# Optimization experiments

Hardware: AMD Instinct MI355X
Metric: run time of the kernel (lower is better)

Reference implementation:

```python
import jax, jax.numpy as jnp
import numpy as np

N = 250_000
E = 8_000_000
EPS = 1e-5


def _bn(x, gamma, beta):
    # BatchNorm1d in training mode: batch stats over dim 0, biased variance
    mu = x.mean(axis=0)
    var = x.var(axis=0)
    return (x - mu) * jax.lax.rsqrt(var + EPS) * gamma + beta


def setup_inputs() -> dict:
    key = jax.random.key(0)
    ks = jax.random.split(key, 24)
    f32 = jnp.float32
    inp = {
        'pos': jax.random.normal(ks[0], (N, 2), f32),
        'vel': jax.random.normal(ks[1], (N, 2), f32),
        'edge_index': jax.random.randint(ks[2], (2, E), 0, N, jnp.int32),
        'lin_in_w': jax.random.normal(ks[3], (4, 4), f32) * 0.5,
        'lin_in_b': jax.random.normal(ks[4], (4,), f32) * 0.1,
        'msg_w1': jax.random.normal(ks[5], (8, 8), f32) * 0.35,
        'msg_b1': jax.random.normal(ks[6], (8,), f32) * 0.1,
        'msg_g1': jax.random.uniform(ks[7], (8,), f32, 0.5, 1.5),
        'msg_be1': jax.random.normal(ks[8], (8,), f32) * 0.1,
        'msg_w2': jax.random.normal(ks[9], (8, 4), f32) * 0.35,
        'msg_b2': jax.random.normal(ks[10], (4,), f32) * 0.1,
        'msg_g2': jax.random.uniform(ks[11], (4,), f32, 0.5, 1.5),
        'msg_be2': jax.random.normal(ks[12], (4,), f32) * 0.1,
        'upd_w1': jax.random.normal(ks[13], (8, 8), f32) * 0.35,
        'upd_b1': jax.random.normal(ks[14], (8,), f32) * 0.1,
        'upd_g1': jax.random.uniform(ks[15], (8,), f32, 0.5, 1.5),
        'upd_be1': jax.random.normal(ks[16], (8,), f32) * 0.1,
        'upd_w2': jax.random.normal(ks[17], (8, 4), f32) * 0.35,
        'upd_b2': jax.random.normal(ks[18], (4,), f32) * 0.1,
        'upd_g2': jax.random.uniform(ks[19], (4,), f32, 0.5, 1.5),
        'upd_be2': jax.random.normal(ks[20], (4,), f32) * 0.1,
        'pred_w': jax.random.normal(ks[21], (4, 2), f32) * 0.5,
        'pred_b': jax.random.normal(ks[22], (2,), f32) * 0.1,
    }
    return inp


def reference(pos, vel, edge_index,
              lin_in_w, lin_in_b,
              msg_w1, msg_b1, msg_g1, msg_be1,
              msg_w2, msg_b2, msg_g2, msg_be2,
              upd_w1, upd_b1, upd_g1, upd_be1,
              upd_w2, upd_b2, upd_g2, upd_be2,
              pred_w, pred_b):
    n = pos.shape[0]
    # input projection: h = lin_in(cat(pos, vel))  -> [N, 4]
    h = jnp.concatenate([pos, vel], axis=-1) @ lin_in_w + lin_in_b

    # PyG source_to_target: j = source = edge_index[0], i = target = edge_index[1]
    src, dst = edge_index[0], edge_index[1]
    h_i = h[dst]  # [E, 4]
    h_j = h[src]  # [E, 4]

    # message MLP on cat(h_i, h_j): Linear->BN->Tanh->Linear->BN->Tanh
    m = jnp.concatenate([h_i, h_j], axis=-1)            # [E, 8]
    m = jnp.tanh(_bn(m @ msg_w1 + msg_b1, msg_g1, msg_be1))
    m = jnp.tanh(_bn(m @ msg_w2 + msg_b2, msg_g2, msg_be2))  # [E, 4]

    # zero out messages where h_i == h_j exactly (self-like edges)
    zero_diff = jnp.all(h_i == h_j, axis=1)             # [E]
    m = jnp.where(zero_diff[:, None], 0.0, m)

    # aggregate: scatter-add on first half, scatter-mean on second half
    add_out = jax.ops.segment_sum(m[:, :2], dst, num_segments=n)   # [N, 2]
    sum_out = jax.ops.segment_sum(m[:, 2:], dst, num_segments=n)   # [N, 2]
    cnt = jax.ops.segment_sum(jnp.ones((m.shape[0],), m.dtype), dst, num_segments=n)
    mean_out = sum_out / jnp.maximum(cnt, 1.0)[:, None]
    aggr = jnp.concatenate([add_out, mean_out], axis=1)  # [N, 4]

    # update MLP on cat(h, aggr)
    u = jnp.concatenate([h, aggr], axis=-1)              # [N, 8]
    u = jnp.tanh(_bn(u @ upd_w1 + upd_b1, upd_g1, upd_be1))
    u = jnp.tanh(_bn(u @ upd_w2 + upd_b2, upd_g2, upd_be2))  # [N, 4]

    return u @ pred_w + pred_b                           # [N, 2]
```

## Files before the change

### kernel.cpp

```cpp
#include <hip/hip_runtime.h>

#define EPSBN 1e-5f
#define NB 512
#define GB 256
#define CAP 18000

typedef float vf4 __attribute__((ext_vector_type(4)));
typedef _Float16 vh8 __attribute__((ext_vector_type(8)));
typedef _Float16 vh4 __attribute__((ext_vector_type(4)));
typedef unsigned int uint32;

__device__ __forceinline__ float ftanh(float x) {
    float e = __expf(2.0f * x);
    return 1.0f - 2.0f * __builtin_amdgcn_rcpf(e + 1.0f);
}

__device__ __forceinline__ float wave_sum(float v) {
#pragma unroll
    for (int off = 32; off > 0; off >>= 1) v += __shfl_down(v, off);
    return v;
}

__device__ __forceinline__ void z1_of(const float4 hi, const float4 hj,
                                      const float* __restrict__ w, const float* __restrict__ b,
                                      float* z) {
#pragma unroll
    for (int j = 0; j < 8; ++j) {
        z[j] = b[j]
             + hi.x * w[0 * 8 + j] + hi.y * w[1 * 8 + j] + hi.z * w[2 * 8 + j] + hi.w * w[3 * 8 + j]
             + hj.x * w[4 * 8 + j] + hj.y * w[5 * 8 + j] + hj.z * w[6 * 8 + j] + hj.w * w[7 * 8 + j];
    }
}

__device__ __forceinline__ void mat8x4(const float* u, const float* w,
                                       const float* b, float* z) {
#pragma unroll
    for (int c = 0; c < 4; ++c) {
        float t = b[c];
#pragma unroll
        for (int k = 0; k < 8; ++k) t += u[k] * w[k * 4 + c];
        z[c] = t;
    }
}

__device__ __forceinline__ void mat8x8(const float* u, const float* __restrict__ w,
                                       const float* __restrict__ b, float* z) {
#pragma unroll
    for (int j = 0; j < 8; ++j) {
        float t = b[j];
#pragma unroll
        for (int k = 0; k < 8; ++k) t += u[k] * w[k * 8 + j];
        z[j] = t;
    }
}

template <int NV, int NW>
__device__ __forceinline__ void block_reduce_atomics(float* a, float* __restrict__ sums) {
    __shared__ float red[NV * NW];
    int wid = threadIdx.x >> 6, lane = threadIdx.x & 63;
#pragma unroll
    for (int i = 0; i < NV; ++i) {
        float v = wave_sum(a[i]);
        if (lane == 0) red[i * NW + wid] = v;
    }
    __syncthreads();
    if (threadIdx.x < NV) {
        float v = 0.f;
#pragma unroll
        for (int k = 0; k < NW; ++k) v += red[threadIdx.x * NW + k];
        atomicAdd(&sums[threadIdx.x], v);
    }
}

__device__ __forceinline__ void fin_lds(const float* __restrict__ sums,
                                        const float* __restrict__ g, const float* __restrict__ be,
                                        int d, float inv, float* out) {
    int j = threadIdx.x;
    if (j < d) {
        float mu = sums[j] * inv;
        float var = sums[d + j] * inv - mu * mu;
        float s = g[j] * rsqrtf(var + EPSBN);
        out[j] = s;
        out[d + j] = be[j] - mu * s;
    }
    __syncthreads();
}

__device__ __forceinline__ void stats1_edge(float4 hi, float4 hj,
                                            const float* __restrict__ w1, const float* __restrict__ b1,
                                            float* a) {
    float z[8];
    z1_of(hi, hj, w1, b1, z);
#pragma unroll
    for (int j = 0; j < 8; ++j) { a[j] += z[j]; a[8 + j] += z[j] * z[j]; }
}

__device__ __forceinline__ vf4 z2_edge(float4 hi, float4 hj,
                                       const float* __restrict__ w1, const float* __restrict__ b1,
                                       const float* ss1,
                                       const float* __restrict__ w2, const float* __restrict__ b2) {
    float z[8], m1[8], z2[4];
    z1_of(hi, hj, w1, b1, z);
#pragma unroll
    for (int j = 0; j < 8; ++j) m1[j] = ftanh(z[j] * ss1[j] + ss1[8 + j]);
    mat8x4(m1, w2, b2, z2);
    vf4 r = {z2[0], z2[1], z2[2], z2[3]};
    return r;
}

__device__ __forceinline__ void stats2_edge(float4 hi, float4 hj,
                                            const float* __restrict__ w1, const float* __restrict__ b1,
                                            const float* ss1,
                                            const float* __restrict__ w2, const float* __restrict__ b2,
                                            float* a) {
    vf4 q = z2_edge(hi, hj, w1, b1, ss1, w2, b2);
    a[0] += q.x; a[4] += q.x * q.x;
    a[1] += q.y; a[5] += q.y * q.y;
    a[2] += q.z; a[6] += q.z * q.z;
    a[3] += q.w; a[7] += q.w * q.w;
}

__global__ __launch_bounds__(256) void k_h(const float* __restrict__ pos, const float* __restrict__ vel,
                                           const float* __restrict__ w, const float* __restrict__ b,
                                           float4* __restrict__ h, int n) {
    int i = blockIdx.x * blockDim.x + threadIdx.x;
    if (i >= n) return;
    float2 p = ((const float2*)pos)[i];
    float2 v = ((const float2*)vel)[i];
    float o[4];
#pragma unroll
    for (int d = 0; d < 4; ++d)
        o[d] = b[d] + p.x * w[0 * 4 + d] + p.y * w[1 * 4 + d] + v.x * w[2 * 4 + d] + v.y * w[3 * 4 + d];
    h[i] = make_float4(o[0], o[1], o[2], o[3]);
}

__global__ __launch_bounds__(256) void k_zt(const float4* __restrict__ h,
                                            const float* __restrict__ w1, const float* __restrict__ b1,
                                            vf4* __restrict__ zi, vh8* __restrict__ zjH, int n) {
    int i = blockIdx.x * blockDim.x + threadIdx.x;
    if (i >= n) return;
    float4 hv = h[i];
    float zi8[8];
    vh8 hpk;
#pragma unroll
    for (int j = 0; j < 8; ++j) {
        zi8[j] = hv.x * w1[0 * 8 + j] + hv.y * w1[1 * 8 + j] + hv.z * w1[2 * 8 + j] + hv.w * w1[3 * 8 + j];
        float zj = b1[j]
                 + hv.x * w1[4 * 8 + j] + hv.y * w1[5 * 8 + j] + hv.z * w1[6 * 8 + j] + hv.w * w1[7 * 8 + j];
        hpk[j] = (_Float16)zj;
    }
    vf4 a = {zi8[0], zi8[1], zi8[2], zi8[3]};
    vf4 b_ = {zi8[4], zi8[5], zi8[6], zi8[7]};
    zi[2 * (size_t)i] = a; zi[2 * (size_t)i + 1] = b_;
    zjH[i] = hpk;
}

__global__ __launch_bounds__(1024, 1) void k_cnt(const int* __restrict__ idx, const float4* __restrict__ h,
                                                 const float* __restrict__ w1, const float* __restrict__ b1,
                                                 uint32* __restrict__ cntmat, float* __restrict__ sums,
                                                 int E_, int T) {
    __shared__ uint32 hist[NB];
    for (int b = threadIdx.x; b < NB; b += 1024) hist[b] = 0;
    float a[16];
#pragma unroll
    for (int i = 0; i < 16; ++i) a[i] = 0.f;
    __syncthreads();
    int lo = blockIdx.x * T, hi2 = min(E_, lo + T);
    for (int e0 = lo + 4 * threadIdx.x; e0 < hi2; e0 += 4096) {
        int m = min(4, hi2 - e0);
        if (m == 4) {
            int s0 = __builtin_nontemporal_load(idx + e0);
            int s1 = __builtin_nontemporal_load(idx + e0 + 1);
            int s2 = __builtin_nontemporal_load(idx + e0 + 2);
            int s3 = __builtin_nontemporal_load(idx + e0 + 3);
            int d0 = __builtin_nontemporal_load(idx + E_ + e0);
            int d1 = __builtin_nontemporal_load(idx + E_ + e0 + 1);
            int d2 = __builtin_nontemporal_load(idx + E_ + e0 + 2);
            int d3 = __builtin_nontemporal_load(idx + E_ + e0 + 3);
            float4 hi0 = h[d0], hj0 = h[s0];
            float4 hi1 = h[d1], hj1 = h[s1];
            float4 hi2 = h[d2], hj2 = h[s2];
            float4 hi3 = h[d3], hj3 = h[s3];
            atomicAdd(&hist[d0 >> 9], 1u);
            atomicAdd(&hist[d1 >> 9], 1u);
            atomicAdd(&hist[d2 >> 9], 1u);
            atomicAdd(&hist[d3 >> 9], 1u);
            stats1_edge(hi0, hj0, w1, b1, a);
            stats1_edge(hi1, hj1, w1, b1, a);
            stats1_edge(hi2, hj2, w1, b1, a);
            stats1_edge(hi3, hj3, w1, b1, a);
        } else {
            for (int k = 0; k < m; ++k) {
                int s = __builtin_nontemporal_load(idx + e0 + k);
                int d = __builtin_nontemporal_load(idx + E_ + e0 + k);
                float4 hi = h[d], hj = h[s];
                atomicAdd(&hist[d >> 9], 1u);
                stats1_edge(hi, hj, w1, b1, a);
            }
        }
    }
    __syncthreads();
    for (int b = threadIdx.x; b < NB; b += 1024)
        cntmat[(size_t)b * GB + blockIdx.x] = hist[b];
    block_reduce_atomics<16, 16>(a, sums);
}

__device__ __forceinline__ void scan256(uint32 v, uint32* excl_out, uint32* total) {
    __shared__ uint32 ts[256];
    ts[threadIdx.x] = v;
    __syncthreads();
    for (int off = 1; off < 256; off <<= 1) {
        uint32 t = (threadIdx.x >= (uint32)off) ? ts[threadIdx.x - off] : 0u;
        __syncthreads();
        ts[threadIdx.x] += t;
        __syncthreads();
    }
    *excl_out = ts[threadIdx.x] - v;
    *total = ts[255];
}

__device__ __forceinline__ void scan512(uint32* v, uint32* excl_out, uint32* total) {
    __shared__ uint32 ts[256];
    uint32 local = v[0] + v[1];
    ts[threadIdx.x] = local;
    __syncthreads();
    for (int off = 1; off < 256; off <<= 1) {
        uint32 t = (threadIdx.x >= (uint32)off) ? ts[threadIdx.x - off] : 0u;
        __syncthreads();
        ts[threadIdx.x] += t;
        __syncthreads();
    }
    *excl_out = ts[threadIdx.x] - local;
    *total = ts[255];
}

__global__ __launch_bounds__(256) void k_scanA(uint32* __restrict__ cntmat, uint32* __restrict__ rowtot) {
    size_t base = (size_t)blockIdx.x * GB + threadIdx.x;
    uint32 v = cntmat[base];
    uint32 excl, tot;
    scan256(v, &excl, &tot);
    cntmat[base] = excl;
    if (threadIdx.x == 0) rowtot[blockIdx.x] = tot;
}

__global__ __launch_bounds__(256) void k_scanB(const uint32* __restrict__ rowtot, uint32* __restrict__ bbase) {
    uint32 v[2];
    v[0] = rowtot[threadIdx.x * 2]; v[1] = rowtot[threadIdx.x * 2 + 1];
    uint32 excl, tot;
    scan512(v, &excl, &tot);
    bbase[threadIdx.x * 2] = excl;
    bbase[threadIdx.x * 2 + 1] = excl + v[0];
    if (threadIdx.x == 0) bbase[NB] = tot;
}

__global__ __launch_bounds__(1024, 1) void k_reorder(const int* __restrict__ idx,
                                                     const uint32* __restrict__ cntmat, const uint32* __restrict__ bbase,
                                                     uint32* __restrict__ sp, int E_, int T) {
    __shared__ uint32 cur[NB];
    for (int b = threadIdx.x; b < NB; b += 1024)
        cur[b] = bbase[b] + cntmat[(size_t)b * GB + blockIdx.x];
    __syncthreads();
    int lo = blockIdx.x * T, hi2 = min(E_, lo + T);
    for (int e0 = lo + 4 * threadIdx.x; e0 < hi2; e0 += 4096) {
        int m = min(4, hi2 - e0);
        if (m == 4) {
            int s0 = __builtin_nontemporal_load(idx + e0);
            int s1 = __builtin_nontemporal_load(idx + e0 + 1);
            int s2 = __builtin_nontemporal_load(idx + e0 + 2);
            int s3 = __builtin_nontemporal_load(idx + e0 + 3);
            int d0 = __builtin_nontemporal_load(idx + E_ + e0);
            int d1 = __builtin_nontemporal_load(idx + E_ + e0 + 1);
            int d2 = __builtin_nontemporal_load(idx + E_ + e0 + 2);
            int d3 = __builtin_nontemporal_load(idx + E_ + e0 + 3);
            uint32 p0 = atomicAdd(&cur[d0 >> 9], 1u);
            uint32 p1 = atomicAdd(&cur[d1 >> 9], 1u);
            uint32 p2 = atomicAdd(&cur[d2 >> 9], 1u);
            uint32 p3 = atomicAdd(&cur[d3 >> 9], 1u);
            sp[p0] = ((uint32)(d0 & 511) << 23) | (uint32)s0;
            sp[p1] = ((uint32)(d1 & 511) << 23) | (uint32)s1;
            sp[p2] = ((uint32)(d2 & 511) << 23) | (uint32)s2;
            sp[p3] = ((uint32)(d3 & 511) << 23) | (uint32)s3;
        } else {
            for (int k = 0; k < m; ++k) {
                int s = __builtin_nontemporal_load(idx + e0 + k);
                int d = __builtin_nontemporal_load(idx + E_ + e0 + k);
                uint32 pos = atomicAdd(&cur[d >> 9], 1u);
                sp[pos] = ((uint32)(d & 511) << 23) | (uint32)s;
            }
        }
    }
}

__global__ __launch_bounds__(256) void k_sort2(const uint32* __restrict__ sp,
                                               const uint32* __restrict__ bbase, const uint32* __restrict__ rowtot,
                                               int* __restrict__ src2, uint32* __restrict__ nodeoff, int n) {
    extern __shared__ uint32 buf[];
    __shared__ uint32 hist[512];
    __shared__ uint32 cur[512];
    int b = blockIdx.x;
    uint32 start = bbase[b];
    uint32 len = rowtot[b];
    uint32 end = start + len;
    hist[threadIdx.x] = 0;
    hist[threadIdx.x + 256] = 0;
    __syncthreads();
    for (uint32 e = start + threadIdx.x; e < end; e += 256) {
        uint32 pk = __builtin_nontemporal_load(&sp[e]);
        atomicAdd(&hist[pk >> 23], 1u);
    }
    __syncthreads();
    uint32 vv[2];
    vv[0] = hist[2 * threadIdx.x];
    vv[1] = hist[2 * threadIdx.x + 1];
    uint32 excl, tot;
    scan512(vv, &excl, &tot);
    cur[2 * threadIdx.x] = excl;
    cur[2 * threadIdx.x + 1] = excl + vv[0];
    int nodebase = b << 9;
    int node0 = nodebase + 2 * threadIdx.x;
    if (node0 <= n)     nodeoff[node0] = start + excl;
    if (node0 + 1 <= n) nodeoff[node0 + 1] = start + excl + vv[0];
    __syncthreads();
    for (uint32 e = start + threadIdx.x; e < end; e += 256) {
        uint32 pk = __builtin_nontemporal_load(&sp[e]);
        uint32 pos = atomicAdd(&cur[pk >> 23], 1u);
        uint32 src = pk & 0x7FFFFFu;
        if (pos < (uint32)CAP) buf[pos] = src;
        else src2[start + pos] = (int)src;
    }
    __syncthreads();
    uint32 lim = min(len, (uint32)CAP);
    for (uint32 k = threadIdx.x; k < lim; k += 256)
        src2[start + k] = (int)buf[k];
}

__global__ void k_fin(const float* __restrict__ sums, float* __restrict__ ss,
                      const float* __restrict__ g, const float* __restrict__ be,
                      int d, float inv_count) {
    int j = threadIdx.x;
    if (j >= d) return;
    float mu = sums[j] * inv_count;
    float var = sums[d + j] * inv_count - mu * mu;
    float s = g[j] * rsqrtf(var + EPSBN);
    ss[j] = s;
    ss[d + j] = be[j] - mu * s;
}

__global__ __launch_bounds__(256) void k_fold(vf4* __restrict__ zi, const float* __restrict__ ss1g, int n) {
    __shared__ float s[16];
    if (threadIdx.x < 16) s[threadIdx.x] = ss1g[threadIdx.x];
    __syncthreads();
    int i = blockIdx.x * blockDim.x + threadIdx.x;
    if (i >= n) return;
    vf4 a = zi[2 * (size_t)i], b = zi[2 * (size_t)i + 1];
    a.x = a.x * s[0] + s[8];  a.y = a.y * s[1] + s[9];
    a.z = a.z * s[2] + s[10]; a.w = a.w * s[3] + s[11];
    b.x = b.x * s[4] + s[12]; b.y = b.y * s[5] + s[13];
    b.z = b.z * s[6] + s[14]; b.w = b.w * s[7] + s[15];
    zi[2 * (size_t)i] = a; zi[2 * (size_t)i + 1] = b;
}

__global__ __launch_bounds__(256, 2) void e_pass2(const int* __restrict__ src2, const uint32* __restrict__ nodeoff,
                                                  const vf4* __restrict__ ziS, const vh8* __restrict__ zjH,
                                                  const float* __restrict__ ss1g,
                                                  const float* __restrict__ w2, const float* __restrict__ b2,
                                                  float* __restrict__ sums2, vh4* __restrict__ z2h, int n) {
    __shared__ float w2l[32];
    __shared__ float b2l[4];
    __shared__ float st[8];
    if (threadIdx.x < 32) w2l[threadIdx.x] = w2[threadIdx.x];
    if (threadIdx.x < 4)  b2l[threadIdx.x] = b2[threadIdx.x];
    if (threadIdx.x < 8)  st[threadIdx.x] = ss1g[threadIdx.x];
    __syncthreads();
    float a[8];
#pragma unroll
    for (int i = 0; i < 8; ++i) a[i] = 0.f;
    int lane = threadIdx.x & 15;
    int gid0 = (blockIdx.x * 256 + threadIdx.x) >> 4;
    int gstride = (gridDim.x * 256) >> 4;
    for (int i = gid0; i < n; i += gstride) {
        uint32 e0 = nodeoff[i], e1 = nodeoff[i + 1];
        vf4 ziA = ziS[2 * (size_t)i], ziB = ziS[2 * (size_t)i + 1];
        float zi8[8] = {ziA.x, ziA.y, ziA.z, ziA.w, ziB.x, ziB.y, ziB.z, ziB.w};
        uint32 e = e0 + lane;
        for (; e + 16 < e1; e += 32) {
            int sA = src2[e];
            int sB = src2[e + 16];
            vh8 ja = zjH[sA];
            vh8 jb = zjH[sB];
            float mA[8], mB[8], zA[4], zB[4];
#pragma unroll
            for (int c = 0; c < 8; ++c) {
                mA[c] = ftanh(zi8[c] + st[c] * (float)ja[c]);
                mB[c] = ftanh(zi8[c] + st[c] * (float)jb[c]);
            }
            mat8x4(mA, w2l, b2l, zA);
            mat8x4(mB, w2l, b2l, zB);
#pragma unroll
            for (int c = 0; c < 4; ++c) {
                a[c] += zA[c] + zB[c];
                a[4 + c] += zA[c] * zA[c] + zB[c] * zB[c];
            }
            vh4 pa, pb2;
            pa[0] = (sA == i) ? (_Float16)__builtin_inff() : (_Float16)zA[0];
            pa[1] = (_Float16)zA[1];
            pa[2] = (_Float16)zA[2];
            pa[3] = (_Float16)zA[3];
            pb2[0] = (sB == i) ? (_Float16)__builtin_inff() : (_Float16)zB[0];
            pb2[1] = (_Float16)zB[1];
            pb2[2] = (_Float16)zB[2];
            pb2[3] = (_Float16)zB[3];
            z2h[e] = pa;
            z2h[e + 16] = pb2;
        }
        if (e < e1) {
            int s = src2[e];
            vh8 zjh = zjH[s];
            float m1[8], z2[4];
#pragma unroll
            for (int c = 0; c < 8; ++c)
                m1[c] = ftanh(zi8[c] + st[c] * (float)zjh[c]);
            mat8x4(m1, w2l, b2l, z2);
#pragma unroll
            for (int c = 0; c < 4; ++c) {
                a[c] += z2[c];
                a[4 + c] += z2[c] * z2[c];
            }
            vh4 pk;
            pk[0] = (s == i) ? (_Float16)__builtin_inff() : (_Float16)z2[0];
            pk[1] = (_Float16)z2[1];
            pk[2] = (_Float16)z2[2];
            pk[3] = (_Float16)z2[3];
            z2h[e] = pk;
        }
    }
    block_reduce_atomics<8, 4>(a, sums2);
}

__global__ __launch_bounds__(256, 2) void e_aggr_z(const vh4* __restrict__ z2h, const uint32* __restrict__ nodeoff,
                                                   const float* __restrict__ sums2,
                                                   const float* __restrict__ g2, const float* __restrict__ be2,
                                                   float invE,
                                                   float* __restrict__ acc, int n) {
    __shared__ float ss2[8];
    fin_lds(sums2, g2, be2, 4, invE, ss2);
    int lane = threadIdx.x & 15;
    int gid0 = (blockIdx.x * 256 + threadIdx.x) >> 4;
    int gstride = (gridDim.x * 256) >> 4;
    for (int i = gid0; i < n; i += gstride) {
        uint32 e0 = nodeoff[i], e1 = nodeoff[i + 1];
        float a0 = 0.f, a1 = 0.f, a2 = 0.f, a3 = 0.f;
        uint32 e = e0 + lane;
        for (; e + 16 < e1; e += 32) {
            vh4 pa = z2h[e];
            vh4 pb = z2h[e + 16];
            float za = (float)pa[0];
            float zb = (float)pb[0];
            if (za != __builtin_inff()) {
                a0 += ftanh(za * ss2[0] + ss2[4]);
                a1 += ftanh((float)pa[1] * ss2[1] + ss2[5]);
                a2 += ftanh((float)pa[2] * ss2[2] + ss2[6]);
                a3 += ftanh((float)pa[3] * ss2[3] + ss2[7]);
            }
            if (zb != __builtin_inff()) {
                a0 += ftanh(zb * ss2[0] + ss2[4]);
                a1 += ftanh((float)pb[1] * ss2[1] + ss2[5]);
                a2 += ftanh((float)pb[2] * ss2[2] + ss2[6]);
                a3 += ftanh((float)pb[3] * ss2[3] + ss2[7]);
            }
        }
        if (e < e1) {
            vh4 pk = z2h[e];
            float z0 = (float)pk[0];
            if (z0 != __builtin_inff()) {
                a0 += ftanh(z0 * ss2[0] + ss2[4]);
                a1 += ftanh((float)pk[1] * ss2[1] + ss2[5]);
                a2 += ftanh((float)pk[2] * ss2[2] + ss2[6]);
                a3 += ftanh((float)pk[3] * ss2[3] + ss2[7]);
            }
        }
#pragma unroll
        for (int off = 8; off > 0; off >>= 1) {
            a0 += __shfl_down(a0, off, 16);
            a1 += __shfl_down(a1, off, 16);
            a2 += __shfl_down(a2, off, 16);
            a3 += __shfl_down(a3, off, 16);
        }
        if (lane == 0) {
            float* ap = acc + 8 * (size_t)i;
            ap[0] = a0; ap[1] = a1; ap[2] = a2; ap[3] = a3;
            ap[4] = (float)(e1 - e0);
        }
    }
}

__global__ __launch_bounds__(256) void fb_stats1(const int* __restrict__ idx, const float4* __restrict__ h,
                                                 const float* __restrict__ w1, const float* __restrict__ b1,
                                                 float* __restrict__ sums, float* __restrict__ acc, int E_) {
    float a[16];
#pragma unroll
    for (int i = 0; i < 16; ++i) a[i] = 0.f;
    int stride = gridDim.x * blockDim.x;
    for (int e = blockIdx.x * blockDim.x + threadIdx.x; e < E_; e += stride) {
        int s = __builtin_nontemporal_load(idx + e);
        int d = __builtin_nontemporal_load(idx + E_ + e);
        float4 hi = h[d], hj = h[s];
        stats1_edge(hi, hj, w1, b1, a);
        atomicAdd(acc + 8 * (size_t)d + 4, 1.0f);
    }
    block_reduce_atomics<16, 4>(a, sums);
}

__global__ __launch_bounds__(256) void fb_stats2(const int* __restrict__ idx, const float4* __restrict__ h,
                                                 const float* __restrict__ w1, const float* __restrict__ b1,
                                                 const float* __restrict__ ss1,
                                                 const float* __restrict__ w2, const float* __restrict__ b2,
                                                 float* __restrict__ sums2, int E_) {
    float a[8];
#pragma unroll
    for (int i = 0; i < 8; ++i) a[i] = 0.f;
    int stride = gridDim.x * blockDim.x;
    for (int e = blockIdx.x * blockDim.x + threadIdx.x; e < E_; e += stride) {
        int s = __builtin_nontemporal_load(idx + e);
        int d = __builtin_nontemporal_load(idx + E_ + e);
        float4 hi = h[d], hj = h[s];
        stats2_edge(hi, hj, w1, b1, ss1, w2, b2, a);
    }
    block_reduce_atomics<8, 4>(a, sums2);
}

__global__ __launch_bounds__(256) void fb_scatter(const int* __restrict__ idx, const float4* __restrict__ h,
                                                  const float* __restrict__ w1, const float* __restrict__ b1,
                                                  const float* __restrict__ ss1,
                                                  const float* __restrict__ w2, const float* __restrict__ b2,
                                                  const float* __restrict__ ss2,
                                                  float* __restrict__ acc, int E_) {
    int stride = gridDim.x * blockDim.x;
    for (int e = blockIdx.x * blockDim.x + threadIdx.x; e < E_; e += stride) {
        int s = __builtin_nontemporal_load(idx + e);
        int d = __builtin_nontemporal_load(idx + E_ + e);
        float4 hi = h[d], hj = h[s];
        bool zero = (hi.x == hj.x) && (hi.y == hj.y) && (hi.z == hj.z) && (hi.w == hj.w);
        if (zero) continue;
        vf4 q = z2_edge(hi, hj, w1, b1, ss1, w2, b2);
        float m0 = ftanh(q.x * ss2[0] + ss2[4]);
        float m1v = ftanh(q.y * ss2[1] + ss2[5]);
        float m2v = ftanh(q.z * ss2[2] + ss2[6]);
        float m3 = ftanh(q.w * ss2[3] + ss2[7]);
        float* ap = acc + 8 * (size_t)d;
        atomicAdd(ap + 0, m0);
        atomicAdd(ap + 1, m1v);
        atomicAdd(ap + 2, m2v);
        atomicAdd(ap + 3, m3);
    }
}

__device__ __forceinline__ void load_u(int i, const float4* __restrict__ h,
                                       const float* __restrict__ acc, float* u) {
    float4 hv = h[i];
    const float* ap = acc + 8 * (size_t)i;
    float c = fmaxf(ap[4], 1.0f);
    u[0] = hv.x; u[1] = hv.y; u[2] = hv.z; u[3] = hv.w;
    u[4] = ap[0]; u[5] = ap[1]; u[6] = ap[2] / c; u[7] = ap[3] / c;
}

__global__ __launch_bounds__(256) void n_stats1(const float4* __restrict__ h,
                                                const float* __restrict__ acc,
                                                const float* __restrict__ w, const float* __restrict__ b,
                                                float* __restrict__ sums, int n) {
    float a[16];
#pragma unroll
    for (int i = 0; i < 16; ++i) a[i] = 0.f;
    int stride = gridDim.x * blockDim.x;
    for (int i = blockIdx.x * blockDim.x + threadIdx.x; i < n; i += stride) {
        float u[8], z[8];
        load_u(i, h, acc, u);
        mat8x8(u, w, b, z);
#pragma unroll
        for (int j = 0; j < 8; ++j) { a[j] += z[j]; a[8 + j] += z[j] * z[j]; }
    }
    block_reduce_atomics<16, 4>(a, sums);
}

__global__ __launch_bounds__(256) void n_stats2(const float4* __restrict__ h,
                                                const float* __restrict__ acc,
                                                const float* __restrict__ w1, const float* __restrict__ b1,
                                                const float* __restrict__ sums3,
                                                const float* __restrict__ g3, const float* __restrict__ be3,
                                                float invN,
                                                const float* __restrict__ w2, const float* __restrict__ b2,
                                                float* __restrict__ sums, int n) {
    __shared__ float ss3[16];
    fin_lds(sums3, g3, be3, 8, invN, ss3);
    float a[8];
#pragma unroll
    for (int i = 0; i < 8; ++i) a[i] = 0.f;
    int stride = gridDim.x * blockDim.x;
    for (int i = blockIdx.x * blockDim.x + threadIdx.x; i < n; i += stride) {
        float u[8], z[8], u1[8], z4[4];
        load_u(i, h, acc, u);
        mat8x8(u, w1, b1, z);
#pragma unroll
        for (int j = 0; j < 8; ++j) u1[j] = ftanh(z[j] * ss3[j] + ss3[8 + j]);
        mat8x4(u1, w2, b2, z4);
#pragma unroll
        for (int c = 0; c < 4; ++c) { a[c] += z4[c]; a[4 + c] += z4[c] * z4[c]; }
    }
    block_reduce_atomics<8, 4>(a, sums);
}

__global__ __launch_bounds__(256) void n_final(const float4* __restrict__ h,
                                               const float* __restrict__ acc,
                                               const float* __restrict__ w1, const float* __restrict__ b1,
                                               const float* __restrict__ sums3,
                                               const float* __restrict__ g3, const float* __restrict__ be3,
                                               const float* __restrict__ sums4,
                                               const float* __restrict__ g4, const float* __restrict__ be4,
                                               float invN,
                                               const float* __restrict__ w2, const float* __restrict__ b2,
                                               const float* __restrict__ pw, const float* __restrict__ pb,
                                               float2* __restrict__ out, int n) {
    __shared__ float ss3[16];
    __shared__ float ss4[8];
    fin_lds(sums3, g3, be3, 8, invN, ss3);
    fin_lds(sums4, g4, be4, 4, invN, ss4);
    int stride = gridDim.x * blockDim.x;
    for (int i = blockIdx.x * blockDim.x + threadIdx.x; i < n; i += stride) {
        float u[8], z[8], u1[8], z4[4], u2[4];
        load_u(i, h, acc, u);
        mat8x8(u, w1, b1, z);
#pragma unroll
        for (int j = 0; j < 8; ++j) u1[j] = ftanh(z[j] * ss3[j] + ss3[8 + j]);
        mat8x4(u1, w2, b2, z4);
#pragma unroll
        for (int c = 0; c < 4; ++c) u2[c] = ftanh(z4[c] * ss4[c] + ss4[4 + c]);
        float o0 = pb[0] + u2[0] * pw[0] + u2[1] * pw[2] + u2[2] * pw[4] + u2[3] * pw[6];
        float o1 = pb[1] + u2[0] * pw[1] + u2[1] * pw[3] + u2[2] * pw[5] + u2[3] * pw[7];
        out[i] = make_float2(o0, o1);
    }
}

extern "C" void kernel_launch(void* const* d_in, const int* in_sizes, int n_in,
                              void* d_out, int out_size, void* d_ws, size_t ws_size,
                              hipStream_t stream) {
    const float* pos  = (const float*)d_in[0];
    const float* vel  = (const float*)d_in[1];
    const int*   eidx = (const int*)d_in[2];
    const float* lin_w = (const float*)d_in[3];
    const float* lin_b = (const float*)d_in[4];
    const float* mw1 = (const float*)d_in[5];
    const float* mb1 = (const float*)d_in[6];
    const float* mg1 = (const float*)d_in[7];
    const float* mbe1 = (const float*)d_in[8];
    const float* mw2 = (const float*)d_in[9];
    const float* mb2 = (const float*)d_in[10];
    const float* mg2 = (const float*)d_in[11];
    const float* mbe2 = (const float*)d_in[12];
    const float* uw1 = (const float*)d_in[13];
    const float* ub1 = (const float*)d_in[14];
    const float* ug1 = (const float*)d_in[15];
    const float* ube1 = (const float*)d_in[16];
    const float* uw2 = (const float*)d_in[17];
    const float* ub2 = (const float*)d_in[18];
    const float* ug2 = (const float*)d_in[19];
    const float* ube2 = (const float*)d_in[20];
    const float* pw = (const float*)d_in[21];
    const float* pb = (const float*)d_in[22];

    int n  = in_sizes[0] / 2;
    int E_ = in_sizes[2] / 2;
    float invE = 1.0f / (float)E_;
    float invN = 1.0f / (float)n;

    char* base = (char*)d_ws;
    size_t off = 0;
    auto alloc = [&](size_t bytes) {
        off = (off + 15) & ~(size_t)15;
        void* p = base + off;
        off += bytes;
        return p;
    };
    float4* h       = (float4*)alloc(16 * (size_t)n);
    float*  acc     = (float*)alloc(32 * (size_t)n);
    float*  sums    = (float*)alloc(512);
    float*  ss      = sums + 64;
    float*  ss1g    = (float*)alloc(256);
    uint32* bbase   = (uint32*)alloc(4 * (NB + 1));
    uint32* rowtot  = (uint32*)alloc(4 * NB);
    uint32* cntmat  = (uint32*)alloc(4 * (size_t)NB * GB);
    uint32* nodeoff = (uint32*)alloc(4 * ((size_t)n + 1));
    vf4*    ziS     = (vf4*)alloc(32 * (size_t)n);
    vh8*    zjH     = (vh8*)alloc(16 * (size_t)n);
    int*    src2    = (int*)alloc(4 * (size_t)E_);
    uint32* sp      = (uint32*)alloc(4 * (size_t)E_);
    vh4*    z2h     = (vh4*)alloc(8 * (size_t)E_);
    size_t need_sort = off;

    bool big = (ws_size >= need_sort) && (n < (1 << 23));

    int nblk = (n + 255) / 256;
    int nbuckets = (n + 511) >> 9;
    int T = (E_ + GB - 1) / GB;

    k_h<<<nblk, 256, 0, stream>>>(pos, vel, lin_w, lin_b, h, n);

    if (big) {
        (void)hipMemsetAsync(sums, 0, 256, stream);

        k_zt<<<nblk, 256, 0, stream>>>(h, mw1, mb1, ziS, zjH, n);

        k_cnt<<<GB, 1024, 0, stream>>>(eidx, h, mw1, mb1, cntmat, sums, E_, T);
        k_scanA<<<NB, 256, 0, stream>>>(cntmat, rowtot);
        k_scanB<<<1, 256, 0, stream>>>(rowtot, bbase);

        k_fin<<<1, 64, 0, stream>>>(sums, ss1g, mg1, mbe1, 8, invE);
        k_fold<<<nblk, 256, 0, stream>>>(ziS, ss1g, n);

        k_reorder<<<GB, 1024, 0, stream>>>(eidx, cntmat, bbase, sp, E_, T);
        k_sort2<<<nbuckets, 256, CAP * 4, stream>>>(sp, bbase, rowtot, src2, nodeoff, n);

        e_pass2<<<4096, 256, 0, stream>>>(src2, nodeoff, ziS, zjH, ss1g,
                                          mw2, mb2, sums + 16, z2h, n);

        e_aggr_z<<<4096, 256, 0, stream>>>(z2h, nodeoff, sums + 16, mg2, mbe2, invE, acc, n);

        n_stats1<<<nblk, 256, 0, stream>>>(h, acc, uw1, ub1, sums + 24, n);
        n_stats2<<<nblk, 256, 0, stream>>>(h, acc, uw1, ub1, sums + 24, ug1, ube1, invN,
                                           uw2, ub2, sums + 40, n);
        n_final<<<nblk, 256, 0, stream>>>(h, acc, uw1, ub1, sums + 24, ug1, ube1,
                                          sums + 40, ug2, ube2, invN,
                                          uw2, ub2, pw, pb, (float2*)d_out, n);
    } else {
        (void)hipMemsetAsync(acc, 0, 32 * (size_t)n + 256, stream);

        fb_stats1<<<4096, 256, 0, stream>>>(eidx, h, mw1, mb1, sums, acc, E_);
        k_fin<<<1, 64, 0, stream>>>(sums, ss, mg1, mbe1, 8, invE);

        fb_stats2<<<4096, 256, 0, stream>>>(eidx, h, mw1, mb1, ss, mw2, mb2, sums + 16, E_);
        k_fin<<<1, 64, 0, stream>>>(sums + 16, ss + 16, mg2, mbe2, 4, invE);

        fb_scatter<<<4096, 256, 0, stream>>>(eidx, h, mw1, mb1, ss, mw2, mb2, ss + 16, acc, E_);

        n_stats1<<<nblk, 256, 0, stream>>>(h, acc, uw1, ub1, sums + 24, n);
        n_stats2<<<nblk, 256, 0, stream>>>(h, acc, uw1, ub1, sums + 24, ug1, ube1, invN,
                                           uw2, ub2, sums + 40, n);
        n_final<<<nblk, 256, 0, stream>>>(h, acc, uw1, ub1, sums + 24, ug1, ube1,
                                          sums + 40, ug2, ube2, invN,
                                          uw2, ub2, pw, pb, (float2*)d_out, n);
    }
}
```

Measured before the change: 414.4 us.

## Fuse per-bucket counting sort with second message layer into one kernel

```diff
diff --git a/kernel.cpp b/kernel.cpp
--- a/kernel.cpp
+++ b/kernel.cpp
@@ -3,7 +3,6 @@
 #define EPSBN 1e-5f
 #define NB 512
 #define GB 256
-#define CAP 18000
 
 typedef float vf4 __attribute__((ext_vector_type(4)));
 typedef _Float16 vh8 __attribute__((ext_vector_type(8)));
@@ -291,49 +290,6 @@
     }
 }
 
-__global__ __launch_bounds__(256) void k_sort2(const uint32* __restrict__ sp,
-                                               const uint32* __restrict__ bbase, const uint32* __restrict__ rowtot,
-                                               int* __restrict__ src2, uint32* __restrict__ nodeoff, int n) {
-    extern __shared__ uint32 buf[];
-    __shared__ uint32 hist[512];
-    __shared__ uint32 cur[512];
-    int b = blockIdx.x;
-    uint32 start = bbase[b];
-    uint32 len = rowtot[b];
-    uint32 end = start + len;
-    hist[threadIdx.x] = 0;
-    hist[threadIdx.x + 256] = 0;
-    __syncthreads();
-    for (uint32 e = start + threadIdx.x; e < end; e += 256) {
-        uint32 pk = __builtin_nontemporal_load(&sp[e]);
-        atomicAdd(&hist[pk >> 23], 1u);
-    }
-    __syncthreads();
-    uint32 vv[2];
-    vv[0] = hist[2 * threadIdx.x];
-    vv[1] = hist[2 * threadIdx.x + 1];
-    uint32 excl, tot;
-    scan512(vv, &excl, &tot);
-    cur[2 * threadIdx.x] = excl;
-    cur[2 * threadIdx.x + 1] = excl + vv[0];
-    int nodebase = b << 9;
-    int node0 = nodebase + 2 * threadIdx.x;
-    if (node0 <= n)     nodeoff[node0] = start + excl;
-    if (node0 + 1 <= n) nodeoff[node0 + 1] = start + excl + vv[0];
-    __syncthreads();
-    for (uint32 e = start + threadIdx.x; e < end; e += 256) {
-        uint32 pk = __builtin_nontemporal_load(&sp[e]);
-        uint32 pos = atomicAdd(&cur[pk >> 23], 1u);
-        uint32 src = pk & 0x7FFFFFu;
-        if (pos < (uint32)CAP) buf[pos] = src;
-        else src2[start + pos] = (int)src;
-    }
-    __syncthreads();
-    uint32 lim = min(len, (uint32)CAP);
-    for (uint32 k = threadIdx.x; k < lim; k += 256)
-        src2[start + k] = (int)buf[k];
-}
-
 __global__ void k_fin(const float* __restrict__ sums, float* __restrict__ ss,
                       const float* __restrict__ g, const float* __restrict__ be,
                       int d, float inv_count) {
@@ -360,81 +316,131 @@
     zi[2 * (size_t)i] = a; zi[2 * (size_t)i + 1] = b;
 }
 
-__global__ __launch_bounds__(256, 2) void e_pass2(const int* __restrict__ src2, const uint32* __restrict__ nodeoff,
+__global__ __launch_bounds__(512, 4) void k_sortz(const uint32* __restrict__ sp,
+                                                  const uint32* __restrict__ bbase, const uint32* __restrict__ rowtot,
                                                   const vf4* __restrict__ ziS, const vh8* __restrict__ zjH,
                                                   const float* __restrict__ ss1g,
                                                   const float* __restrict__ w2, const float* __restrict__ b2,
-                                                  float* __restrict__ sums2, vh4* __restrict__ z2h, int n) {
+                                                  float* __restrict__ sums2, vh4* __restrict__ z2h,
+                                                  uint32* __restrict__ nodeoff, int n) {
+    __shared__ uint32 hist[512];
+    __shared__ uint32 cur[512];
+    __shared__ uint32 ts[256];
     __shared__ float w2l[32];
     __shared__ float b2l[4];
     __shared__ float st[8];
+    int b = blockIdx.x;
+    uint32 start = bbase[b];
+    uint32 len = rowtot[b];
+    uint32 end = start + len;
+    int nb9 = b << 9;
+
+    hist[threadIdx.x] = 0;
     if (threadIdx.x < 32) w2l[threadIdx.x] = w2[threadIdx.x];
     if (threadIdx.x < 4)  b2l[threadIdx.x] = b2[threadIdx.x];
     if (threadIdx.x < 8)  st[threadIdx.x] = ss1g[threadIdx.x];
     __syncthreads();
+
+    for (uint32 e = start + threadIdx.x; e < end; e += 512) {
+        uint32 pk = __builtin_nontemporal_load(&sp[e]);
+        atomicAdd(&hist[pk >> 23], 1u);
+    }
+    __syncthreads();
+
+    uint32 v0 = 0, v1 = 0;
+    if (threadIdx.x < 256) {
+        v0 = hist[2 * threadIdx.x];
+        v1 = hist[2 * threadIdx.x + 1];
+        ts[threadIdx.x] = v0 + v1;
+    }
+    __syncthreads();
+    for (int off = 1; off < 256; off <<= 1) {
+        uint32 t = 0;
+        if (threadIdx.x < 256 && threadIdx.x >= (uint32)off) t = ts[threadIdx.x - off];
+        __syncthreads();
+        if (threadIdx.x < 256) ts[threadIdx.x] += t;
+        __syncthreads();
+    }
+    if (threadIdx.x < 256) {
+        uint32 excl = ts[threadIdx.x] - v0 - v1;
+        cur[2 * threadIdx.x] = excl;
+        cur[2 * threadIdx.x + 1] = excl + v0;
+        int node0 = nb9 + 2 * (int)threadIdx.x;
+        if (node0 <= n)     nodeoff[node0] = start + excl;
+        if (node0 + 1 <= n) nodeoff[node0 + 1] = start + excl + v0;
+    }
+    __syncthreads();
+
     float a[8];
 #pragma unroll
     for (int i = 0; i < 8; ++i) a[i] = 0.f;
-    int lane = threadIdx.x & 15;
-    int gid0 = (blockIdx.x * 256 + threadIdx.x) >> 4;
-    int gstride = (gridDim.x * 256) >> 4;
-    for (int i = gid0; i < n; i += gstride) {
-        uint32 e0 = nodeoff[i], e1 = nodeoff[i + 1];
-        vf4 ziA = ziS[2 * (size_t)i], ziB = ziS[2 * (size_t)i + 1];
-        float zi8[8] = {ziA.x, ziA.y, ziA.z, ziA.w, ziB.x, ziB.y, ziB.z, ziB.w};
-        uint32 e = e0 + lane;
-        for (; e + 16 < e1; e += 32) {
-            int sA = src2[e];
-            int sB = src2[e + 16];
-            vh8 ja = zjH[sA];
-            vh8 jb = zjH[sB];
-            float mA[8], mB[8], zA[4], zB[4];
-#pragma unroll
-            for (int c = 0; c < 8; ++c) {
-                mA[c] = ftanh(zi8[c] + st[c] * (float)ja[c]);
-                mB[c] = ftanh(zi8[c] + st[c] * (float)jb[c]);
-            }
-            mat8x4(mA, w2l, b2l, zA);
-            mat8x4(mB, w2l, b2l, zB);
-#pragma unroll
-            for (int c = 0; c < 4; ++c) {
-                a[c] += zA[c] + zB[c];
-                a[4 + c] += zA[c] * zA[c] + zB[c] * zB[c];
-            }
-            vh4 pa, pb2;
-            pa[0] = (sA == i) ? (_Float16)__builtin_inff() : (_Float16)zA[0];
-            pa[1] = (_Float16)zA[1];
-            pa[2] = (_Float16)zA[2];
-            pa[3] = (_Float16)zA[3];
-            pb2[0] = (sB == i) ? (_Float16)__builtin_inff() : (_Float16)zB[0];
-            pb2[1] = (_Float16)zB[1];
-            pb2[2] = (_Float16)zB[2];
-            pb2[3] = (_Float16)zB[3];
-            z2h[e] = pa;
-            z2h[e + 16] = pb2;
-        }
-        if (e < e1) {
-            int s = src2[e];
-            vh8 zjh = zjH[s];
-            float m1[8], z2[4];
-#pragma unroll
-            for (int c = 0; c < 8; ++c)
-                m1[c] = ftanh(zi8[c] + st[c] * (float)zjh[c]);
-            mat8x4(m1, w2l, b2l, z2);
-#pragma unroll
-            for (int c = 0; c < 4; ++c) {
-                a[c] += z2[c];
-                a[4 + c] += z2[c] * z2[c];
-            }
-            vh4 pk;
-            pk[0] = (s == i) ? (_Float16)__builtin_inff() : (_Float16)z2[0];
-            pk[1] = (_Float16)z2[1];
-            pk[2] = (_Float16)z2[2];
-            pk[3] = (_Float16)z2[3];
-            z2h[e] = pk;
-        }
-    }
-    block_reduce_atomics<8, 4>(a, sums2);
+    uint32 e = start + threadIdx.x;
+    for (; e + 512 < end; e += 1024) {
+        uint32 pkA = __builtin_nontemporal_load(&sp[e]);
+        uint32 pkB = __builtin_nontemporal_load(&sp[e + 512]);
+        int lA = pkA >> 23, lB = pkB >> 23;
+        int sA = pkA & 0x7FFFFF, sB = pkB & 0x7FFFFF;
+        size_t nA = (size_t)(nb9 + lA), nB2 = (size_t)(nb9 + lB);
+        vf4 ziA0 = ziS[2 * nA], ziA1 = ziS[2 * nA + 1];
+        vf4 ziB0 = ziS[2 * nB2], ziB1 = ziS[2 * nB2 + 1];
+        vh8 ja = zjH[sA];
+        vh8 jb = zjH[sB];
+        uint32 pA = atomicAdd(&cur[lA], 1u);
+        uint32 pB = atomicAdd(&cur[lB], 1u);
+        float zAi[8] = {ziA0.x, ziA0.y, ziA0.z, ziA0.w, ziA1.x, ziA1.y, ziA1.z, ziA1.w};
+        float zBi[8] = {ziB0.x, ziB0.y, ziB0.z, ziB0.w, ziB1.x, ziB1.y, ziB1.z, ziB1.w};
+        float mA[8], mB[8], zA[4], zB[4];
+#pragma unroll
+        for (int c = 0; c < 8; ++c) {
+            mA[c] = ftanh(zAi[c] + st[c] * (float)ja[c]);
+            mB[c] = ftanh(zBi[c] + st[c] * (float)jb[c]);
+        }
+        mat8x4(mA, w2l, b2l, zA);
+        mat8x4(mB, w2l, b2l, zB);
+#pragma unroll
+        for (int c = 0; c < 4; ++c) {
+            a[c] += zA[c] + zB[c];
+            a[4 + c] += zA[c] * zA[c] + zB[c] * zB[c];
+        }
+        vh4 qa, qb;
+        qa[0] = (sA == nb9 + lA) ? (_Float16)__builtin_inff() : (_Float16)zA[0];
+        qa[1] = (_Float16)zA[1];
+        qa[2] = (_Float16)zA[2];
+        qa[3] = (_Float16)zA[3];
+        qb[0] = (sB == nb9 + lB) ? (_Float16)__builtin_inff() : (_Float16)zB[0];
+        qb[1] = (_Float16)zB[1];
+        qb[2] = (_Float16)zB[2];
+        qb[3] = (_Float16)zB[3];
+        z2h[start + pA] = qa;
+        z2h[start + pB] = qb;
+    }
+    if (e < end) {
+        uint32 pk = __builtin_nontemporal_load(&sp[e]);
+        int local = pk >> 23;
+        int s = pk & 0x7FFFFF;
+        size_t ni = (size_t)(nb9 + local);
+        vf4 zi0 = ziS[2 * ni], zi1 = ziS[2 * ni + 1];
+        vh8 zjh = zjH[s];
+        uint32 pos = atomicAdd(&cur[local], 1u);
+        float zi8[8] = {zi0.x, zi0.y, zi0.z, zi0.w, zi1.x, zi1.y, zi1.z, zi1.w};
+        float m1[8], z2[4];
+#pragma unroll
+        for (int c = 0; c < 8; ++c)
+            m1[c] = ftanh(zi8[c] + st[c] * (float)zjh[c]);
+        mat8x4(m1, w2l, b2l, z2);
+#pragma unroll
+        for (int c = 0; c < 4; ++c) {
+            a[c] += z2[c];
+            a[4 + c] += z2[c] * z2[c];
+        }
+        vh4 pk4;
+        pk4[0] = (s == nb9 + local) ? (_Float16)__builtin_inff() : (_Float16)z2[0];
+        pk4[1] = (_Float16)z2[1];
+        pk4[2] = (_Float16)z2[2];
+        pk4[3] = (_Float16)z2[3];
+        z2h[start + pos] = pk4;
+    }
+    block_reduce_atomics<8, 8>(a, sums2);
 }
 
 __global__ __launch_bounds__(256, 2) void e_aggr_z(const vh4* __restrict__ z2h, const uint32* __restrict__ nodeoff,
@@ -691,7 +697,6 @@
     uint32* nodeoff = (uint32*)alloc(4 * ((size_t)n + 1));
     vf4*    ziS     = (vf4*)alloc(32 * (size_t)n);
     vh8*    zjH     = (vh8*)alloc(16 * (size_t)n);
-    int*    src2    = (int*)alloc(4 * (size_t)E_);
     uint32* sp      = (uint32*)alloc(4 * (size_t)E_);
     vh4*    z2h     = (vh4*)alloc(8 * (size_t)E_);
     size_t need_sort = off;
@@ -717,10 +722,9 @@
         k_fold<<<nblk, 256, 0, stream>>>(ziS, ss1g, n);
 
         k_reorder<<<GB, 1024, 0, stream>>>(eidx, cntmat, bbase, sp, E_, T);
-        k_sort2<<<nbuckets, 256, CAP * 4, stream>>>(sp, bbase, rowtot, src2, nodeoff, n);
-
-        e_pass2<<<4096, 256, 0, stream>>>(src2, nodeoff, ziS, zjH, ss1g,
-                                          mw2, mb2, sums + 16, z2h, n);
+
+        k_sortz<<<nbuckets, 512, 0, stream>>>(sp, bbase, rowtot, ziS, zjH, ss1g,
+                                              mw2, mb2, sums + 16, z2h, nodeoff, n);
 
         e_aggr_z<<<4096, 256, 0, stream>>>(z2h, nodeoff, sums + 16, mg2, mbe2, invE, acc, n);
 
```

Measured after the change: 512.7 us. +23.7%, slower.
